# Kernel optimization log

Hardware: AMD Instinct MI355X
Metric: run time of the kernel (lower is better)

The kernel has to match this reference:

```python
import jax, jax.numpy as jnp
import numpy as np

B, S, D, E = 2, 2048, 512, 8
H = 4 * D


def setup_inputs() -> dict:
    key = jax.random.key(0)
    ks = jax.random.split(key, 7)
    x = jax.random.normal(ks[0], (B, S, D), jnp.float32)
    Wg = jax.random.normal(ks[1], (D, E), jnp.float32) * (D ** -0.5)
    bg = jnp.zeros((E,), jnp.float32)
    W1 = jax.random.normal(ks[2], (E, D, H), jnp.float32) * (D ** -0.5)
    b1 = jnp.zeros((E, H), jnp.float32)
    W2 = jax.random.normal(ks[3], (E, H, D), jnp.float32) * (H ** -0.5)
    b2 = jnp.zeros((E, D), jnp.float32)
    return {"x": x, "Wg": Wg, "bg": bg, "W1": W1, "b1": b1, "W2": W2, "b2": b2}


def reference(x, Wg, bg, W1, b1, W2, b2):
    b, s, d = x.shape
    xt = x.reshape(-1, d)                       # [T, d]
    T = xt.shape[0]
    n_experts = Wg.shape[1]
    route_probs = jax.nn.softmax(xt @ Wg + bg, axis=1)   # [T, E]
    route_max_val = route_probs.max(axis=1)              # [T]
    route_max_ind = route_probs.argmax(axis=1)           # [T] int
    # Run every expert on all tokens, then select per-token winner
    h = jax.nn.relu(jnp.einsum('td,edh->eth', xt, W1) + b1[:, None, :])   # [E,T,4d]
    y_all = jnp.einsum('eth,ehd->etd', h, W2) + b2[:, None, :]            # [E,T,d]
    outputs = y_all[route_max_ind, jnp.arange(T)] * route_max_val[:, None]
    # Load-balancing loss (faithful to original indexing quirk):
    # fi is a length-T vector whose first E entries are per-expert counts / T
    counts = jax.ops.segment_sum(jnp.ones((T,), xt.dtype), route_max_ind,
                                 num_segments=n_experts)
    fi = jnp.zeros((T,), xt.dtype).at[:n_experts].set(counts) / T
    pi = route_probs.mean(axis=1)                         # [T], == 1/E per row
    load_balancing_loss = 0.01 * n_experts * jnp.dot(fi, pi)
    return outputs.reshape(b, s, d), load_balancing_loss
```

## Files before the change

### kernel.cpp

```cpp
#include <hip/hip_runtime.h>
#include <hip/hip_bf16.h>
#include <cstddef>
#include <cstdint>


namespace {

constexpr int T = 4096;
constexpr int D = 512;
constexpr int E = 8;
constexpr int H = 2048;

typedef __attribute__((ext_vector_type(8))) short short8;
typedef __attribute__((ext_vector_type(4))) float f32x4;

struct WS {
  int   counts[8];
  int   base[8];
  float pi8[8];
  float rv[T];
  int   ridx[T];
  int   list[T];
};

constexpr size_t HDR     = (sizeof(WS) + 255) & ~size_t(255);
constexpr size_t XB_OFF  = HDR;
constexpr size_t WT1_OFF = XB_OFF  + 2 * (size_t)T * D;
constexpr size_t WT2_OFF = WT1_OFF + 2 * (size_t)E * H * D;
constexpr size_t HB_OFF  = WT2_OFF + 2 * (size_t)E * D * H;

#define GLD16(g, l)                                                       \
  __builtin_amdgcn_global_load_lds(                                       \
      (const __attribute__((address_space(1))) void*)(g),                 \
      (__attribute__((address_space(3))) void*)(l), 16, 0, 0)

__global__ __launch_bounds__(256) void route_k(const float* __restrict__ x,
                                               const float* __restrict__ Wg,
                                               const float* __restrict__ bg,
                                               __hip_bfloat16* __restrict__ xb,
                                               WS* __restrict__ ws) {
  const int wave = threadIdx.x >> 6;
  const int lane = threadIdx.x & 63;
  const int t = blockIdx.x * 4 + wave;
  const float* xr = x + (size_t)t * D;

  const float4* xp = reinterpret_cast<const float4*>(xr) + lane * 2;
  float4 a = xp[0], b4 = xp[1];
  float xs[8] = {a.x, a.y, a.z, a.w, b4.x, b4.y, b4.z, b4.w};
  alignas(16) __hip_bfloat16 o[8];
#pragma unroll
  for (int j = 0; j < 8; ++j) o[j] = __float2bfloat16(xs[j]);
  *reinterpret_cast<int4*>(xb + (size_t)t * D + lane * 8) = *reinterpret_cast<int4*>(o);

  float acc[8] = {0.f, 0.f, 0.f, 0.f, 0.f, 0.f, 0.f, 0.f};
#pragma unroll
  for (int i = 0; i < 8; ++i) {
    const int k = lane * 8 + i;
    const float4* w = reinterpret_cast<const float4*>(Wg + (size_t)k * 8);
    float4 w0 = w[0], w1 = w[1];
    float xv = xs[i];
    acc[0] += xv * w0.x; acc[1] += xv * w0.y; acc[2] += xv * w0.z; acc[3] += xv * w0.w;
    acc[4] += xv * w1.x; acc[5] += xv * w1.y; acc[6] += xv * w1.z; acc[7] += xv * w1.w;
  }

#pragma unroll
  for (int j = 0; j < 4; ++j) {
    float send = (lane & 1) ? acc[j] : acc[j + 4];
    float recv = __shfl_xor(send, 1, 64);
    acc[j] = ((lane & 1) ? acc[j + 4] : acc[j]) + recv;
  }
#pragma unroll
  for (int j = 0; j < 2; ++j) {
    float send = (lane & 2) ? acc[j] : acc[j + 2];
    float recv = __shfl_xor(send, 2, 64);
    acc[j] = ((lane & 2) ? acc[j + 2] : acc[j]) + recv;
  }
  {
    float send = (lane & 4) ? acc[0] : acc[1];
    float recv = __shfl_xor(send, 4, 64);
    acc[0] = ((lane & 4) ? acc[1] : acc[0]) + recv;
  }
  float v = acc[0];
  v += __shfl_xor(v, 8, 64);
  v += __shfl_xor(v, 16, 64);
  v += __shfl_xor(v, 32, 64);
  const int e = 4 * (lane & 1) + 2 * ((lane >> 1) & 1) + ((lane >> 2) & 1);

  float lg = v + bg[e];
  float m = lg;
  m = fmaxf(m, __shfl_xor(m, 1, 64));
  m = fmaxf(m, __shfl_xor(m, 2, 64));
  m = fmaxf(m, __shfl_xor(m, 4, 64));
  float p = expf(lg - m);
  float s = p;
  s += __shfl_xor(s, 1, 64);
  s += __shfl_xor(s, 2, 64);
  s += __shfl_xor(s, 4, 64);
  float pr = p / s;
  float psum = pr;
  psum += __shfl_xor(psum, 1, 64);
  psum += __shfl_xor(psum, 2, 64);
  psum += __shfl_xor(psum, 4, 64);
  unsigned long long key =
      ((unsigned long long)__float_as_uint(pr) << 8) | (unsigned)(7 - e);
  unsigned long long k2;
  k2 = __shfl_xor(key, 1, 64); key = key > k2 ? key : k2;
  k2 = __shfl_xor(key, 2, 64); key = key > k2 ? key : k2;
  k2 = __shfl_xor(key, 4, 64); key = key > k2 ? key : k2;

  if (lane == 0) {
    int ebest = 7 - (int)(key & 0xffull);
    float prmax = __uint_as_float((unsigned)(key >> 8));
    ws->rv[t] = prmax;
    ws->ridx[t] = ebest;
    if (t < 8) ws->pi8[t] = psum * 0.125f;
  }
}

__global__ __launch_bounds__(1024) void plan_k(WS* __restrict__ ws,
                                               float* __restrict__ out) {
  __shared__ int lcnt[8];
  __shared__ int lbase[8];
  const int tid = threadIdx.x;
  if (tid < 8) lcnt[tid] = 0;
  __syncthreads();
  int mye[4], mypos[4];
#pragma unroll
  for (int i = 0; i < 4; ++i) {
    int e = ws->ridx[tid + i * 1024];
    mye[i] = e;
    mypos[i] = atomicAdd(&lcnt[e], 1);
  }
  __syncthreads();
  if (tid == 0) {
    int b = 0;
    float s = 0.f;
#pragma unroll
    for (int e = 0; e < 8; ++e) {
      int c = lcnt[e];
      ws->counts[e] = c;
      ws->base[e] = b;
      lbase[e] = b;
      b += c;
      s += ((float)c / (float)T) * ws->pi8[e];
    }
    out[(size_t)T * D] = 0.01f * (float)E * s;
  }
  __syncthreads();
#pragma unroll
  for (int i = 0; i < 4; ++i)
    ws->list[lbase[mye[i]] + mypos[i]] = tid + i * 1024;
}

template <int K, int N>
__global__ __launch_bounds__(256) void cvt_t(const float* __restrict__ in,
                                             __hip_bfloat16* __restrict__ outp) {
  const int e = blockIdx.z;
  in   += (size_t)e * K * N;
  outp += (size_t)e * K * N;
  const int k0 = blockIdx.y * 64, n0 = blockIdx.x * 64;
  __shared__ __hip_bfloat16 tile[64][72];
  const int r = threadIdx.x >> 4, c = (threadIdx.x & 15) * 4;
#pragma unroll
  for (int rr = 0; rr < 4; ++rr) {
    float4 v = *reinterpret_cast<const float4*>(in + (size_t)(k0 + r + rr * 16) * N + n0 + c);
    tile[r + rr * 16][c + 0] = __float2bfloat16(v.x);
    tile[r + rr * 16][c + 1] = __float2bfloat16(v.y);
    tile[r + rr * 16][c + 2] = __float2bfloat16(v.z);
    tile[r + rr * 16][c + 3] = __float2bfloat16(v.w);
  }
  __syncthreads();
  const int n = threadIdx.x >> 2, ch = threadIdx.x & 3;
  alignas(16) __hip_bfloat16 o[16];
#pragma unroll
  for (int i = 0; i < 16; ++i) o[i] = tile[ch * 16 + i][n];
  __hip_bfloat16* dst = outp + (size_t)(n0 + n) * K + k0 + ch * 16;
  reinterpret_cast<int4*>(dst)[0] = reinterpret_cast<int4*>(o)[0];
  reinterpret_cast<int4*>(dst)[1] = reinterpret_cast<int4*>(o)[1];
}

template <int K, int BN, int WR, int WC, bool SECOND>
__global__ __launch_bounds__(256) void mgemm(const __hip_bfloat16* __restrict__ Ag,
                                             const __hip_bfloat16* __restrict__ Wt,
                                             const float* __restrict__ bias,
                                             __hip_bfloat16* __restrict__ hb,
                                             float* __restrict__ outp,
                                             WS* __restrict__ ws) {
  constexpr int BM = 128;
  constexpr int BK = 64;
  constexpr int NDIM = SECOND ? D : H;
  constexpr int MS = BM / WR, NS = BN / WC;
  constexpr int MF = MS / 16, NF = NS / 16;
  constexpr int ACALLS = BM / 32;
  constexpr int BCALLS = BN / 32;

  const int e = blockIdx.z;
  const int cnt = ws->counts[e];
  const int m0 = blockIdx.y * BM;
  if (m0 >= cnt) return;
  const int n0 = blockIdx.x * BN;
  const int bas = ws->base[e];
  const int* lst = ws->list + bas;

  const int tid = threadIdx.x, lane = tid & 63, wave = tid >> 6;
  const int wr = wave / WC, wc = wave % WC;
  const int wrow = wr * MS, wcol = wc * NS;

  __shared__ unsigned char As[BM * 128];
  __shared__ unsigned char Bs[BN * 128];

  const int srow = tid >> 3;
  const int sj = tid & 7;
  const unsigned short* aptr[ACALLS];
#pragma unroll
  for (int q = 0; q < ACALLS; ++q) {
    int row = q * 32 + srow;
    int jj = sj ^ (row & 7);
    int mrow = m0 + row; if (mrow > cnt - 1) mrow = cnt - 1;
    int arow = SECOND ? (bas + mrow) : lst[mrow];
    aptr[q] = reinterpret_cast<const unsigned short*>(Ag) + (size_t)arow * K + jj * 8;
  }
  const unsigned short* bptr[BCALLS];
#pragma unroll
  for (int q = 0; q < BCALLS; ++q) {
    int row = q * 32 + srow;
    int jj = sj ^ (row & 7);
    bptr[q] = reinterpret_cast<const unsigned short*>(Wt) +
              ((size_t)e * NDIM + n0 + row) * K + jj * 8;
  }

  f32x4 acc[MF][NF] = {};

  for (int k0 = 0; k0 < K; k0 += BK) {
#pragma unroll
    for (int q = 0; q < ACALLS; ++q) GLD16(aptr[q] + k0, As + q * 4096 + (wave << 10));
#pragma unroll
    for (int q = 0; q < BCALLS; ++q) GLD16(bptr[q] + k0, Bs + q * 4096 + (wave << 10));
    __syncthreads();
#pragma unroll
    for (int s = 0; s < 2; ++s) {
      const int jA = s * 4 + (lane >> 4);
      short8 af[MF], bfr[NF];
#pragma unroll
      for (int m = 0; m < MF; ++m) {
        int row = wrow + m * 16 + (lane & 15);
        af[m] = *reinterpret_cast<const short8*>(As + row * 128 + ((jA ^ (row & 7)) << 4));
      }
#pragma unroll
      for (int n = 0; n < NF; ++n) {
        int row = wcol + n * 16 + (lane & 15);
        bfr[n] = *reinterpret_cast<const short8*>(Bs + row * 128 + ((jA ^ (row & 7)) << 4));
      }
#pragma unroll
      for (int m = 0; m < MF; ++m)
#pragma unroll
        for (int n = 0; n < NF; ++n)
          acc[m][n] = __builtin_amdgcn_mfma_f32_16x16x32_bf16(af[m], bfr[n], acc[m][n], 0, 0, 0);
    }
    __syncthreads();
  }

  const int colbase = n0 + wcol + (lane & 15);
  float bia[NF];
#pragma unroll
  for (int n = 0; n < NF; ++n) bia[n] = bias[(size_t)e * NDIM + colbase + n * 16];
#pragma unroll
  for (int m = 0; m < MF; ++m) {
    const int rloc = wrow + m * 16 + ((lane >> 4) << 2);
#pragma unroll
    for (int i = 0; i < 4; ++i) {
      const int r = m0 + rloc + i;
      if (r < cnt) {
        if (!SECOND) {
          __hip_bfloat16* hrow = hb + (size_t)(bas + r) * H + colbase;
#pragma unroll
          for (int n = 0; n < NF; ++n)
            hrow[n * 16] = __float2bfloat16(fmaxf(acc[m][n][i] + bia[n], 0.f));
        } else {
          const int t = lst[r];
          const float s = ws->rv[t];
          float* orow = outp + (size_t)t * D + colbase;
#pragma unroll
          for (int n = 0; n < NF; ++n)
            orow[n * 16] = (acc[m][n][i] + bia[n]) * s;
        }
      }
    }
  }
}

}

extern "C" void kernel_launch(void* const* d_in, const int* in_sizes, int n_in,
                              void* d_out, int out_size, void* d_ws, size_t ws_size,
                              hipStream_t stream) {
  const float* x  = (const float*)d_in[0];
  const float* Wg = (const float*)d_in[1];
  const float* bg = (const float*)d_in[2];
  const float* W1 = (const float*)d_in[3];
  const float* b1 = (const float*)d_in[4];
  const float* W2 = (const float*)d_in[5];
  const float* b2 = (const float*)d_in[6];
  float* out = (float*)d_out;
  WS* ws = (WS*)d_ws;
  char* wsb = (char*)d_ws;
  __hip_bfloat16* xb  = (__hip_bfloat16*)(wsb + XB_OFF);
  __hip_bfloat16* wt1 = (__hip_bfloat16*)(wsb + WT1_OFF);
  __hip_bfloat16* wt2 = (__hip_bfloat16*)(wsb + WT2_OFF);
  __hip_bfloat16* hbp = (__hip_bfloat16*)(wsb + HB_OFF);

  hipLaunchKernelGGL(route_k, dim3(T / 4), dim3(256), 0, stream, x, Wg, bg, xb, ws);
  hipLaunchKernelGGL(plan_k, dim3(1), dim3(1024), 0, stream, ws, out);
  hipLaunchKernelGGL((cvt_t<D, H>), dim3(H / 64, D / 64, E), dim3(256), 0, stream, W1, wt1);
  hipLaunchKernelGGL((cvt_t<H, D>), dim3(D / 64, H / 64, E), dim3(256), 0, stream, W2, wt2);
  hipLaunchKernelGGL((mgemm<D, 128, 2, 2, false>), dim3(H / 128, 32, E), dim3(256), 0, stream,
                     xb, wt1, b1, hbp, nullptr, ws);
  hipLaunchKernelGGL((mgemm<H, 64, 4, 1, true>), dim3(D / 64, 32, E), dim3(256), 0, stream,
                     hbp, wt2, b2, nullptr, out, ws);
}
```

Baseline: 200.1 us.

## Split-K second expert GEMM with atomic accumulation and smaller M tiles

The second GEMM now splits K in two and accumulates scaled partial results into the output with atomic adds. A new prefill kernel initialises the output with the routed bias times the gate value. Both GEMMs use 64-row M tiles so more blocks are launched across the uneven per-expert token counts. The weight transpose kernel now keeps fp32 in shared memory and converts on readout. The aim is better occupancy and load balance, at the cost of atomic traffic, an extra pass over the output, and a non-deterministic summation order.

```diff
diff --git a/kernel.cpp b/kernel.cpp
--- a/kernel.cpp
+++ b/kernel.cpp
@@ -152,6 +152,20 @@
     ws->list[lbase[mye[i]] + mypos[i]] = tid + i * 1024;
 }
 
+__global__ __launch_bounds__(256) void prefill_k(const float* __restrict__ b2,
+                                                 const WS* __restrict__ ws,
+                                                 float* __restrict__ out) {
+  const int idx = blockIdx.x * 256 + threadIdx.x;
+  const int t = idx >> 7;
+  const int d = (idx & 127) * 4;
+  const float rvv = ws->rv[t];
+  const int e = ws->ridx[t];
+  float4 b = *reinterpret_cast<const float4*>(b2 + (size_t)e * D + d);
+  float4 r;
+  r.x = b.x * rvv; r.y = b.y * rvv; r.z = b.z * rvv; r.w = b.w * rvv;
+  *reinterpret_cast<float4*>(out + (size_t)t * D + d) = r;
+}
+
 template <int K, int N>
 __global__ __launch_bounds__(256) void cvt_t(const float* __restrict__ in,
                                              __hip_bfloat16* __restrict__ outp) {
@@ -159,42 +173,43 @@
   in   += (size_t)e * K * N;
   outp += (size_t)e * K * N;
   const int k0 = blockIdx.y * 64, n0 = blockIdx.x * 64;
-  __shared__ __hip_bfloat16 tile[64][72];
+  __shared__ float tile[64][65];
   const int r = threadIdx.x >> 4, c = (threadIdx.x & 15) * 4;
 #pragma unroll
   for (int rr = 0; rr < 4; ++rr) {
     float4 v = *reinterpret_cast<const float4*>(in + (size_t)(k0 + r + rr * 16) * N + n0 + c);
-    tile[r + rr * 16][c + 0] = __float2bfloat16(v.x);
-    tile[r + rr * 16][c + 1] = __float2bfloat16(v.y);
-    tile[r + rr * 16][c + 2] = __float2bfloat16(v.z);
-    tile[r + rr * 16][c + 3] = __float2bfloat16(v.w);
+    tile[r + rr * 16][c + 0] = v.x;
+    tile[r + rr * 16][c + 1] = v.y;
+    tile[r + rr * 16][c + 2] = v.z;
+    tile[r + rr * 16][c + 3] = v.w;
   }
   __syncthreads();
-  const int n = threadIdx.x >> 2, ch = threadIdx.x & 3;
+  const int n = threadIdx.x >> 2, kc = threadIdx.x & 3;
   alignas(16) __hip_bfloat16 o[16];
 #pragma unroll
-  for (int i = 0; i < 16; ++i) o[i] = tile[ch * 16 + i][n];
-  __hip_bfloat16* dst = outp + (size_t)(n0 + n) * K + k0 + ch * 16;
+  for (int i = 0; i < 16; ++i) o[i] = __float2bfloat16(tile[kc * 16 + i][n]);
+  __hip_bfloat16* dst = outp + (size_t)(n0 + n) * K + k0 + kc * 16;
   reinterpret_cast<int4*>(dst)[0] = reinterpret_cast<int4*>(o)[0];
   reinterpret_cast<int4*>(dst)[1] = reinterpret_cast<int4*>(o)[1];
 }
 
-template <int K, int BN, int WR, int WC, bool SECOND>
+template <int K, int BM, int BN, int WR, int WC, int KSPLIT, bool SECOND>
 __global__ __launch_bounds__(256) void mgemm(const __hip_bfloat16* __restrict__ Ag,
                                              const __hip_bfloat16* __restrict__ Wt,
                                              const float* __restrict__ bias,
                                              __hip_bfloat16* __restrict__ hb,
                                              float* __restrict__ outp,
                                              WS* __restrict__ ws) {
-  constexpr int BM = 128;
   constexpr int BK = 64;
   constexpr int NDIM = SECOND ? D : H;
   constexpr int MS = BM / WR, NS = BN / WC;
   constexpr int MF = MS / 16, NF = NS / 16;
   constexpr int ACALLS = BM / 32;
   constexpr int BCALLS = BN / 32;
-
-  const int e = blockIdx.z;
+  constexpr int KCH = K / KSPLIT;
+
+  const int e = blockIdx.z / KSPLIT;
+  const int kz = blockIdx.z % KSPLIT;
   const int cnt = ws->counts[e];
   const int m0 = blockIdx.y * BM;
   if (m0 >= cnt) return;
@@ -231,7 +246,7 @@
 
   f32x4 acc[MF][NF] = {};
 
-  for (int k0 = 0; k0 < K; k0 += BK) {
+  for (int k0 = kz * KCH; k0 < (kz + 1) * KCH; k0 += BK) {
 #pragma unroll
     for (int q = 0; q < ACALLS; ++q) GLD16(aptr[q] + k0, As + q * 4096 + (wave << 10));
 #pragma unroll
@@ -262,8 +277,10 @@
 
   const int colbase = n0 + wcol + (lane & 15);
   float bia[NF];
-#pragma unroll
-  for (int n = 0; n < NF; ++n) bia[n] = bias[(size_t)e * NDIM + colbase + n * 16];
+  if (!SECOND) {
+#pragma unroll
+    for (int n = 0; n < NF; ++n) bia[n] = bias[(size_t)e * NDIM + colbase + n * 16];
+  }
 #pragma unroll
   for (int m = 0; m < MF; ++m) {
     const int rloc = wrow + m * 16 + ((lane >> 4) << 2);
@@ -278,11 +295,11 @@
             hrow[n * 16] = __float2bfloat16(fmaxf(acc[m][n][i] + bia[n], 0.f));
         } else {
           const int t = lst[r];
-          const float s = ws->rv[t];
+          const float sc = ws->rv[t];
           float* orow = outp + (size_t)t * D + colbase;
 #pragma unroll
           for (int n = 0; n < NF; ++n)
-            orow[n * 16] = (acc[m][n][i] + bia[n]) * s;
+            unsafeAtomicAdd(orow + n * 16, acc[m][n][i] * sc);
         }
       }
     }
@@ -311,10 +328,11 @@
 
   hipLaunchKernelGGL(route_k, dim3(T / 4), dim3(256), 0, stream, x, Wg, bg, xb, ws);
   hipLaunchKernelGGL(plan_k, dim3(1), dim3(1024), 0, stream, ws, out);
+  hipLaunchKernelGGL(prefill_k, dim3(T * D / 1024), dim3(256), 0, stream, b2, ws, out);
   hipLaunchKernelGGL((cvt_t<D, H>), dim3(H / 64, D / 64, E), dim3(256), 0, stream, W1, wt1);
   hipLaunchKernelGGL((cvt_t<H, D>), dim3(D / 64, H / 64, E), dim3(256), 0, stream, W2, wt2);
-  hipLaunchKernelGGL((mgemm<D, 128, 2, 2, false>), dim3(H / 128, 32, E), dim3(256), 0, stream,
-                     xb, wt1, b1, hbp, nullptr, ws);
-  hipLaunchKernelGGL((mgemm<H, 64, 4, 1, true>), dim3(D / 64, 32, E), dim3(256), 0, stream,
-                     hbp, wt2, b2, nullptr, out, ws);
-}
+  hipLaunchKernelGGL((mgemm<D, 64, 128, 2, 2, 1, false>), dim3(H / 128, T / 64, E),
+                     dim3(256), 0, stream, xb, wt1, b1, hbp, nullptr, ws);
+  hipLaunchKernelGGL((mgemm<H, 64, 64, 2, 2, 2, true>), dim3(D / 64, T / 64, E * 2),
+                     dim3(256), 0, stream, hbp, wt2, b2, nullptr, out, ws);
+}
```

Result: faster. 188.8 us (-5.7%).
